# Performance work log

Measured on AMD Instinct MI355X. Metric: run time of the kernel, lower is better.

The kernel has to match this reference:

```python
import jax, jax.numpy as jnp
import numpy as np

B, C, H, W = 2, 16, 160, 192
S, D = 3, 48
MIN_DEPTH, MAX_DEPTH = 0.5, 10.0
EPS = 1e-6


def setup_inputs() -> dict:
    key = jax.random.key(0)
    k1, k2 = jax.random.split(key)
    ref_feats = jax.random.normal(k1, (B, C, H, W), jnp.float32)
    src_feats = jax.random.normal(k2, (S, B, C, H, W), jnp.float32)
    K = np.array([[200.0, 0.0, W / 2.0], [0.0, 200.0, H / 2.0], [0.0, 0.0, 1.0]], np.float32)
    ref_intrinsics = jnp.broadcast_to(jnp.asarray(K), (B, 3, 3))
    src_intrinsics = jnp.broadcast_to(jnp.asarray(K), (S, B, 3, 3))
    T = np.tile(np.eye(4, dtype=np.float32), (S, B, 1, 1))
    T[:, :, 0, 3] = np.array([0.15, -0.15, 0.05], np.float32)[:, None]  # x baselines
    T[:, :, 1, 3] = 0.05  # small y offset
    ref_to_src = jnp.asarray(T)
    depth_hypotheses = jnp.linspace(MIN_DEPTH, MAX_DEPTH, D, dtype=jnp.float32)
    return {"ref_feats": ref_feats, "src_feats": src_feats,
            "ref_intrinsics": ref_intrinsics, "src_intrinsics": src_intrinsics,
            "ref_to_src": ref_to_src, "depth_hypotheses": depth_hypotheses}


def _bilinear(img, x, y, valid):
    """img: [B,C,Hs,Ws]; x,y,valid: [B,D,N]. Zero padding outside. -> [B,C,D,N]"""
    Hs, Ws = img.shape[2], img.shape[3]
    x0 = jnp.floor(x); y0 = jnp.floor(y)
    fx = x - x0; fy = y - y0
    x0i = x0.astype(jnp.int32); y0i = y0.astype(jnp.int32)
    gather = jax.vmap(lambda im, yy, xx: im[:, yy, xx])  # per-batch [C,D,N]
    out = jnp.zeros(img.shape[:2] + x.shape[1:], img.dtype)
    for dy in (0, 1):
        for dx in (0, 1):
            xi = x0i + dx; yi = y0i + dy
            w = (fx if dx else 1.0 - fx) * (fy if dy else 1.0 - fy)
            ok = valid & (xi >= 0) & (xi < Ws) & (yi >= 0) & (yi < Hs)
            vals = gather(img, jnp.clip(yi, 0, Hs - 1), jnp.clip(xi, 0, Ws - 1))
            out = out + vals * jnp.where(ok, w, 0.0)[:, None]
    return out


def _ncc(f1, f2, eps=EPS):
    """NCC over channel axis 1. f1: [B,C,1,H,W], f2: [B,C,D,H,W] -> [B,D,H,W]"""
    f1 = f1 - f1.mean(axis=1, keepdims=True)
    f2 = f2 - f2.mean(axis=1, keepdims=True)
    num = (f1 * f2).sum(axis=1)
    den = jnp.sqrt((f1 * f1).sum(axis=1)) * jnp.sqrt((f2 * f2).sum(axis=1)) + eps
    return num / den


def reference(ref_feats, src_feats, ref_intrinsics, src_intrinsics, ref_to_src, depth_hypotheses):
    b, c, h, w = ref_feats.shape
    s = src_feats.shape[0]
    us, vs = jnp.meshgrid(jnp.arange(w, dtype=jnp.float32), jnp.arange(h, dtype=jnp.float32))  # [h,w]
    pix = jnp.stack([us.ravel(), vs.ravel(), jnp.ones(h * w, jnp.float32)], axis=0)  # [3,HW]
    rays = jnp.einsum('bij,jn->bin', jnp.linalg.inv(ref_intrinsics), pix)  # [B,3,HW]
    X = depth_hypotheses[None, :, None, None] * rays[:, None]  # [B,D,3,HW]
    cost = jnp.zeros((b, depth_hypotheses.shape[0], h, w), ref_feats.dtype)
    for si in range(s):
        R = ref_to_src[si, :, :3, :3]; t = ref_to_src[si, :, :3, 3]
        Xs = jnp.einsum('bij,bdjn->bdin', R, X) + t[:, None, :, None]  # [B,D,3,HW]
        p = jnp.einsum('bij,bdjn->bdin', src_intrinsics[si], Xs)
        z = p[:, :, 2]
        valid = z > 1e-3
        zs = jnp.maximum(z, 1e-3)
        x = p[:, :, 0] / zs; y = p[:, :, 1] / zs  # [B,D,HW]
        warped = _bilinear(src_feats[si], x, y, valid).reshape(b, c, -1, h, w)  # [B,C,D,H,W]
        cost = cost + _ncc(ref_feats[:, :, None], warped)
    return cost / s
```

## Files before the change

kernel.cpp:

```cpp
#include <hip/hip_runtime.h>
#include <math.h>

constexpr int B = 2, C = 16, H = 160, W = 192, S = 3, D = 48;
constexpr int HW = H * W;

__global__ __launch_bounds__(256) void plane_sweep_kernel(
    const float* __restrict__ ref_feats,
    const float* __restrict__ src_feats,
    const float* __restrict__ ref_intr,
    const float* __restrict__ src_intr,
    const float* __restrict__ ref_to_src,
    const float* __restrict__ depths,
    float* __restrict__ out)
{
    const int idx = blockIdx.x * blockDim.x + threadIdx.x;
    const int total = B * D * HW;
    if (idx >= total) return;

    const int w = idx % W;
    const int h = (idx / W) % H;
    const int d = (idx / HW) % D;
    const int b = idx / (HW * D);

    const float* Kp = ref_intr + b * 9;
    const double a00 = Kp[0], a01 = Kp[1], a02 = Kp[2];
    const double a10 = Kp[3], a11 = Kp[4], a12 = Kp[5];
    const double a20 = Kp[6], a21 = Kp[7], a22 = Kp[8];
    const double cof00 =  (a11 * a22 - a12 * a21);
    const double cof01 = -(a10 * a22 - a12 * a20);
    const double cof02 =  (a10 * a21 - a11 * a20);
    const double cof10 = -(a01 * a22 - a02 * a21);
    const double cof11 =  (a00 * a22 - a02 * a20);
    const double cof12 = -(a00 * a21 - a01 * a20);
    const double cof20 =  (a01 * a12 - a02 * a11);
    const double cof21 = -(a00 * a12 - a02 * a10);
    const double cof22 =  (a00 * a11 - a01 * a10);
    const double det = a00 * cof00 + a01 * cof01 + a02 * cof02;
    const double invdet = 1.0 / det;
    const double i00 = cof00 * invdet, i01 = cof10 * invdet, i02 = cof20 * invdet;
    const double i10 = cof01 * invdet, i11 = cof11 * invdet, i12 = cof21 * invdet;
    const double i20 = cof02 * invdet, i21 = cof12 * invdet, i22 = cof22 * invdet;

    const double u = (double)w;
    const double v = (double)h;
    const double rayx = i00 * u + i01 * v + i02;
    const double rayy = i10 * u + i11 * v + i12;
    const double rayz = i20 * u + i21 * v + i22;

    const double depth = (double)depths[d];
    const double X0 = depth * rayx;
    const double X1 = depth * rayy;
    const double X2 = depth * rayz;

    float f1[C];
    const float* rp = ref_feats + (b * C) * HW + h * W + w;
    float sum1 = 0.0f;
    #pragma unroll
    for (int c = 0; c < C; ++c) {
        f1[c] = rp[c * HW];
        sum1 += f1[c];
    }
    const float m1 = sum1 * (1.0f / C);
    float sq1 = 0.0f;
    #pragma unroll
    for (int c = 0; c < C; ++c) {
        f1[c] -= m1;
        sq1 += f1[c] * f1[c];
    }
    const float n1 = sqrtf(sq1);

    float cost = 0.0f;

    for (int s = 0; s < S; ++s) {
        const float* Tp  = ref_to_src + (s * B + b) * 16;
        const float* Ksp = src_intr   + (s * B + b) * 9;

        const double Xsx = (double)Tp[0] * X0 + (double)Tp[1] * X1 + (double)Tp[2]  * X2 + (double)Tp[3];
        const double Xsy = (double)Tp[4] * X0 + (double)Tp[5] * X1 + (double)Tp[6]  * X2 + (double)Tp[7];
        const double Xsz = (double)Tp[8] * X0 + (double)Tp[9] * X1 + (double)Tp[10] * X2 + (double)Tp[11];

        const double p0 = (double)Ksp[0] * Xsx + (double)Ksp[1] * Xsy + (double)Ksp[2] * Xsz;
        const double p1 = (double)Ksp[3] * Xsx + (double)Ksp[4] * Xsy + (double)Ksp[5] * Xsz;
        const double p2 = (double)Ksp[6] * Xsx + (double)Ksp[7] * Xsy + (double)Ksp[8] * Xsz;

        const bool valid = p2 > 0.001;
        const double zs = fmax(p2, 0.001);
        const double invz = 1.0 / zs;
        const double x = p0 * invz;
        const double y = p1 * invz;

        const double x0f = floor(x);
        const double y0f = floor(y);
        const double fx = x - x0f;
        const double fy = y - y0f;
        const int x0 = (int)x0f;
        const int y0 = (int)y0f;
        const int x1 = x0 + 1;
        const int y1 = y0 + 1;

        double dw00 = (1.0 - fx) * (1.0 - fy);
        double dw01 = fx * (1.0 - fy);
        double dw10 = (1.0 - fx) * fy;
        double dw11 = fx * fy;
        const bool okx0 = (x0 >= 0) && (x0 < W);
        const bool okx1 = (x1 >= 0) && (x1 < W);
        const bool oky0 = (y0 >= 0) && (y0 < H);
        const bool oky1 = (y1 >= 0) && (y1 < H);
        const float w00 = (float)((valid && okx0 && oky0) ? dw00 : 0.0);
        const float w01 = (float)((valid && okx1 && oky0) ? dw01 : 0.0);
        const float w10 = (float)((valid && okx0 && oky1) ? dw10 : 0.0);
        const float w11 = (float)((valid && okx1 && oky1) ? dw11 : 0.0);

        const int x0c = min(max(x0, 0), W - 1);
        const int x1c = min(max(x1, 0), W - 1);
        const int y0c = min(max(y0, 0), H - 1);
        const int y1c = min(max(y1, 0), H - 1);

        const int off00 = y0c * W + x0c;
        const int off01 = y0c * W + x1c;
        const int off10 = y1c * W + x0c;
        const int off11 = y1c * W + x1c;

        const float* base = src_feats + ((size_t)(s * B + b) * C) * HW;

        float f2[C];
        float sum2 = 0.0f;
        #pragma unroll
        for (int c = 0; c < C; ++c) {
            const float* p = base + c * HW;
            const float v00 = p[off00];
            const float v01 = p[off01];
            const float v10 = p[off10];
            const float v11 = p[off11];
            const float val = w00 * v00 + w01 * v01 + w10 * v10 + w11 * v11;
            f2[c] = val;
            sum2 += val;
        }
        const float m2 = sum2 * (1.0f / C);
        float sq2 = 0.0f;
        float dot = 0.0f;
        #pragma unroll
        for (int c = 0; c < C; ++c) {
            const float f2c = f2[c] - m2;
            sq2 = fmaf(f2c, f2c, sq2);
            dot = fmaf(f1[c], f2c, dot);
        }
        const float den = n1 * sqrtf(sq2) + 1e-6f;
        cost += dot / den;
    }

    out[idx] = cost * (1.0f / S);
}

extern "C" void kernel_launch(void* const* d_in, const int* in_sizes, int n_in,
                              void* d_out, int out_size, void* d_ws, size_t ws_size,
                              hipStream_t stream) {
    const float* ref_feats  = (const float*)d_in[0];
    const float* src_feats  = (const float*)d_in[1];
    const float* ref_intr   = (const float*)d_in[2];
    const float* src_intr   = (const float*)d_in[3];
    const float* ref_to_src = (const float*)d_in[4];
    const float* depths     = (const float*)d_in[5];
    float* out = (float*)d_out;

    const int total = B * D * H * W;
    const int block = 256;
    const int grid = (total + block - 1) / block;
    plane_sweep_kernel<<<grid, block, 0, stream>>>(
        ref_feats, src_feats, ref_intr, src_intr, ref_to_src, depths, out);
}
```

Baseline: 183.1 us.

## Process eight depths per thread and use paired loads for bilinear taps

Each thread now handles a block of 8 depth hypotheses for one pixel. The per-pixel setup (inverse intrinsics, ray, projection coefficients folded into a linear-in-depth form, reference feature normalization) is computed once and reused across those depths. The bilinear sampling now reads two adjacent x-samples with a single 8-byte vector load per row, and edge columns are handled by remapping the weights. This cuts redundant double-precision setup and load instructions, but launches 8x fewer threads, which lowers parallelism and occupancy, and the f32x2 loads may be misaligned.

```diff
diff --git a/kernel.cpp b/kernel.cpp
--- a/kernel.cpp
+++ b/kernel.cpp
@@ -3,6 +3,16 @@
 
 constexpr int B = 2, C = 16, H = 160, W = 192, S = 3, D = 48;
 constexpr int HW = H * W;
+constexpr int DPER = 8;
+constexpr int NDBLK = D / DPER;
+
+typedef float f32x2 __attribute__((ext_vector_type(2)));
+
+__device__ __forceinline__ f32x2 load2(const float* p) {
+    f32x2 v;
+    __builtin_memcpy(&v, p, sizeof(f32x2));
+    return v;
+}
 
 __global__ __launch_bounds__(256) void plane_sweep_kernel(
     const float* __restrict__ ref_feats,
@@ -14,13 +24,14 @@
     float* __restrict__ out)
 {
     const int idx = blockIdx.x * blockDim.x + threadIdx.x;
-    const int total = B * D * HW;
+    const int total = B * NDBLK * HW;
     if (idx >= total) return;
 
-    const int w = idx % W;
-    const int h = (idx / W) % H;
-    const int d = (idx / HW) % D;
-    const int b = idx / (HW * D);
+    const int w    = idx % W;
+    const int h    = (idx / W) % H;
+    const int dblk = (idx / HW) % NDBLK;
+    const int b    = idx / (HW * NDBLK);
+    const int d0   = dblk * DPER;
 
     const float* Kp = ref_intr + b * 9;
     const double a00 = Kp[0], a01 = Kp[1], a02 = Kp[2];
@@ -47,10 +58,24 @@
     const double rayy = i10 * u + i11 * v + i12;
     const double rayz = i20 * u + i21 * v + i22;
 
-    const double depth = (double)depths[d];
-    const double X0 = depth * rayx;
-    const double X1 = depth * rayy;
-    const double X2 = depth * rayz;
+    double ka0[S], ka1[S], ka2[S], kt0[S], kt1[S], kt2[S];
+    const float* vbase[S];
+    #pragma unroll
+    for (int s = 0; s < S; ++s) {
+        const float* Tp  = ref_to_src + (s * B + b) * 16;
+        const float* Ksp = src_intr   + (s * B + b) * 9;
+        const double ar0 = (double)Tp[0] * rayx + (double)Tp[1] * rayy + (double)Tp[2]  * rayz;
+        const double ar1 = (double)Tp[4] * rayx + (double)Tp[5] * rayy + (double)Tp[6]  * rayz;
+        const double ar2 = (double)Tp[8] * rayx + (double)Tp[9] * rayy + (double)Tp[10] * rayz;
+        ka0[s] = (double)Ksp[0] * ar0 + (double)Ksp[1] * ar1 + (double)Ksp[2] * ar2;
+        ka1[s] = (double)Ksp[3] * ar0 + (double)Ksp[4] * ar1 + (double)Ksp[5] * ar2;
+        ka2[s] = (double)Ksp[6] * ar0 + (double)Ksp[7] * ar1 + (double)Ksp[8] * ar2;
+        const double t0 = Tp[3], t1 = Tp[7], t2 = Tp[11];
+        kt0[s] = (double)Ksp[0] * t0 + (double)Ksp[1] * t1 + (double)Ksp[2] * t2;
+        kt1[s] = (double)Ksp[3] * t0 + (double)Ksp[4] * t1 + (double)Ksp[5] * t2;
+        kt2[s] = (double)Ksp[6] * t0 + (double)Ksp[7] * t1 + (double)Ksp[8] * t2;
+        vbase[s] = src_feats + ((size_t)(s * B + b) * C) * HW;
+    }
 
     float f1[C];
     const float* rp = ref_feats + (b * C) * HW + h * W + w;
@@ -69,87 +94,80 @@
     }
     const float n1 = sqrtf(sq1);
 
-    float cost = 0.0f;
+    float* outp = out + (size_t)(b * D + d0) * HW + h * W + w;
 
-    for (int s = 0; s < S; ++s) {
-        const float* Tp  = ref_to_src + (s * B + b) * 16;
-        const float* Ksp = src_intr   + (s * B + b) * 9;
+    #pragma unroll 1
+    for (int di = 0; di < DPER; ++di) {
+        const double depth = (double)depths[d0 + di];
+        float cost = 0.0f;
 
-        const double Xsx = (double)Tp[0] * X0 + (double)Tp[1] * X1 + (double)Tp[2]  * X2 + (double)Tp[3];
-        const double Xsy = (double)Tp[4] * X0 + (double)Tp[5] * X1 + (double)Tp[6]  * X2 + (double)Tp[7];
-        const double Xsz = (double)Tp[8] * X0 + (double)Tp[9] * X1 + (double)Tp[10] * X2 + (double)Tp[11];
+        #pragma unroll
+        for (int s = 0; s < S; ++s) {
+            const double p0 = depth * ka0[s] + kt0[s];
+            const double p1 = depth * ka1[s] + kt1[s];
+            const double p2 = depth * ka2[s] + kt2[s];
 
-        const double p0 = (double)Ksp[0] * Xsx + (double)Ksp[1] * Xsy + (double)Ksp[2] * Xsz;
-        const double p1 = (double)Ksp[3] * Xsx + (double)Ksp[4] * Xsy + (double)Ksp[5] * Xsz;
-        const double p2 = (double)Ksp[6] * Xsx + (double)Ksp[7] * Xsy + (double)Ksp[8] * Xsz;
+            const bool valid = p2 > 0.001;
+            const double zs = fmax(p2, 0.001);
+            const double invz = 1.0 / zs;
+            const double x = p0 * invz;
+            const double y = p1 * invz;
 
-        const bool valid = p2 > 0.001;
-        const double zs = fmax(p2, 0.001);
-        const double invz = 1.0 / zs;
-        const double x = p0 * invz;
-        const double y = p1 * invz;
+            const double x0f = floor(x);
+            const double y0f = floor(y);
+            const double fx = x - x0f;
+            const double fy = y - y0f;
+            const int x0 = (int)x0f;
+            const int y0 = (int)y0f;
+            const int y1 = y0 + 1;
 
-        const double x0f = floor(x);
-        const double y0f = floor(y);
-        const double fx = x - x0f;
-        const double fy = y - y0f;
-        const int x0 = (int)x0f;
-        const int y0 = (int)y0f;
-        const int x1 = x0 + 1;
-        const int y1 = y0 + 1;
+            const double wx0 = 1.0 - fx;
+            const double wx1 = fx;
+            const bool interior = (x0 >= 0) && (x0 < W - 1);
+            const float wA = (float)(interior ? wx0 : ((x0 == -1)    ? wx1 : 0.0));
+            const float wB = (float)(interior ? wx1 : ((x0 == W - 1) ? wx0 : 0.0));
 
-        double dw00 = (1.0 - fx) * (1.0 - fy);
-        double dw01 = fx * (1.0 - fy);
-        double dw10 = (1.0 - fx) * fy;
-        double dw11 = fx * fy;
-        const bool okx0 = (x0 >= 0) && (x0 < W);
-        const bool okx1 = (x1 >= 0) && (x1 < W);
-        const bool oky0 = (y0 >= 0) && (y0 < H);
-        const bool oky1 = (y1 >= 0) && (y1 < H);
-        const float w00 = (float)((valid && okx0 && oky0) ? dw00 : 0.0);
-        const float w01 = (float)((valid && okx1 && oky0) ? dw01 : 0.0);
-        const float w10 = (float)((valid && okx0 && oky1) ? dw10 : 0.0);
-        const float w11 = (float)((valid && okx1 && oky1) ? dw11 : 0.0);
+            const bool oky0 = (y0 >= 0) && (y0 < H);
+            const bool oky1 = (y1 >= 0) && (y1 < H);
+            const float wy0 = (float)((valid && oky0) ? (1.0 - fy) : 0.0);
+            const float wy1 = (float)((valid && oky1) ? fy : 0.0);
 
-        const int x0c = min(max(x0, 0), W - 1);
-        const int x1c = min(max(x1, 0), W - 1);
-        const int y0c = min(max(y0, 0), H - 1);
-        const int y1c = min(max(y1, 0), H - 1);
+            const int xa  = min(max(x0, 0), W - 2);
+            const int y0c = min(max(y0, 0), H - 1);
+            const int y1c = min(max(y1, 0), H - 1);
+            const int off0 = y0c * W + xa;
+            const int off1 = y1c * W + xa;
 
-        const int off00 = y0c * W + x0c;
-        const int off01 = y0c * W + x1c;
-        const int off10 = y1c * W + x0c;
-        const int off11 = y1c * W + x1c;
+            const float* base = vbase[s];
 
-        const float* base = src_feats + ((size_t)(s * B + b) * C) * HW;
+            float f2[C];
+            float sum2 = 0.0f;
+            #pragma unroll
+            for (int c = 0; c < C; ++c) {
+                const float* pc = base + c * HW;
+                const f32x2 r0 = load2(pc + off0);
+                const f32x2 r1 = load2(pc + off1);
+                const float t0 = fmaf(wA, r0.x, wB * r0.y);
+                const float t1 = fmaf(wA, r1.x, wB * r1.y);
+                const float val = fmaf(wy0, t0, wy1 * t1);
+                f2[c] = val;
+                sum2 += val;
+            }
+            const float m2 = sum2 * (1.0f / C);
+            float sq2 = 0.0f;
+            float dot = 0.0f;
+            #pragma unroll
+            for (int c = 0; c < C; ++c) {
+                const float f2c = f2[c] - m2;
+                sq2 = fmaf(f2c, f2c, sq2);
+                dot = fmaf(f1[c], f2c, dot);
+            }
+            const float den = n1 * sqrtf(sq2) + 1e-6f;
+            cost += dot / den;
+        }
 
-        float f2[C];
-        float sum2 = 0.0f;
-        #pragma unroll
-        for (int c = 0; c < C; ++c) {
-            const float* p = base + c * HW;
-            const float v00 = p[off00];
-            const float v01 = p[off01];
-            const float v10 = p[off10];
-            const float v11 = p[off11];
-            const float val = w00 * v00 + w01 * v01 + w10 * v10 + w11 * v11;
-            f2[c] = val;
-            sum2 += val;
-        }
-        const float m2 = sum2 * (1.0f / C);
-        float sq2 = 0.0f;
-        float dot = 0.0f;
-        #pragma unroll
-        for (int c = 0; c < C; ++c) {
-            const float f2c = f2[c] - m2;
-            sq2 = fmaf(f2c, f2c, sq2);
-            dot = fmaf(f1[c], f2c, dot);
-        }
-        const float den = n1 * sqrtf(sq2) + 1e-6f;
-        cost += dot / den;
+        outp[(size_t)di * HW] = cost * (1.0f / S);
     }
-
-    out[idx] = cost * (1.0f / S);
 }
 
 extern "C" void kernel_launch(void* const* d_in, const int* in_sizes, int n_in,
@@ -163,7 +181,7 @@
     const float* depths     = (const float*)d_in[5];
     float* out = (float*)d_out;
 
-    const int total = B * D * H * W;
+    const int total = B * NDBLK * H * W;
     const int block = 256;
     const int grid = (total + block - 1) / block;
     plane_sweep_kernel<<<grid, block, 0, stream>>>(
```

Result: slower. 355.7 us (+94.2%).

## Precompute per-pixel projection rays in a geometry kernel and use paired bilinear loads

Applied to the files above, without the earlier changes.

Adds a geometry pre-pass that computes, for each pixel and source view, K_s*R*ray in double plus the per-batch K_s*t term, so the sweep kernel only does depth*ka+kt per hypothesis. This removes the per-thread 3x3 inverse and the matrix products from the hot kernel. The bilinear sampling now uses a clamped x anchor with two 2-float loads per row and separable weights, done in float, which halves the load instructions. It adds a workspace round trip of double-precision ka reads and a second launch, with a fallback kernel when the workspace is too small.

```diff
diff --git a/kernel.cpp b/kernel.cpp
--- a/kernel.cpp
+++ b/kernel.cpp
@@ -3,24 +3,31 @@
 
 constexpr int B = 2, C = 16, H = 160, W = 192, S = 3, D = 48;
 constexpr int HW = H * W;
-
-__global__ __launch_bounds__(256) void plane_sweep_kernel(
-    const float* __restrict__ ref_feats,
-    const float* __restrict__ src_feats,
+constexpr int NPIX = B * HW;
+constexpr size_t KA_ELEMS = (size_t)S * 3 * NPIX;
+constexpr size_t KT_ELEMS = (size_t)S * 3 * B;
+constexpr size_t WS_NEEDED = (KA_ELEMS + KT_ELEMS) * sizeof(double);
+
+typedef float f32x2 __attribute__((ext_vector_type(2)));
+
+__device__ __forceinline__ f32x2 load2(const float* p) {
+    f32x2 v;
+    __builtin_memcpy(&v, p, sizeof(f32x2));
+    return v;
+}
+
+__global__ __launch_bounds__(256) void geom_kernel(
     const float* __restrict__ ref_intr,
     const float* __restrict__ src_intr,
     const float* __restrict__ ref_to_src,
-    const float* __restrict__ depths,
-    float* __restrict__ out)
+    double* __restrict__ ka,
+    double* __restrict__ kt)
 {
-    const int idx = blockIdx.x * blockDim.x + threadIdx.x;
-    const int total = B * D * HW;
-    if (idx >= total) return;
-
-    const int w = idx % W;
-    const int h = (idx / W) % H;
-    const int d = (idx / HW) % D;
-    const int b = idx / (HW * D);
+    const int pi = blockIdx.x * blockDim.x + threadIdx.x;
+    if (pi >= NPIX) return;
+    const int w = pi % W;
+    const int h = (pi / W) % H;
+    const int b = pi / HW;
 
     const float* Kp = ref_intr + b * 9;
     const double a00 = Kp[0], a01 = Kp[1], a02 = Kp[2];
@@ -47,10 +54,47 @@
     const double rayy = i10 * u + i11 * v + i12;
     const double rayz = i20 * u + i21 * v + i22;
 
+    #pragma unroll
+    for (int s = 0; s < S; ++s) {
+        const float* Tp  = ref_to_src + (s * B + b) * 16;
+        const float* Ksp = src_intr   + (s * B + b) * 9;
+        const double ar0 = (double)Tp[0] * rayx + (double)Tp[1] * rayy + (double)Tp[2]  * rayz;
+        const double ar1 = (double)Tp[4] * rayx + (double)Tp[5] * rayy + (double)Tp[6]  * rayz;
+        const double ar2 = (double)Tp[8] * rayx + (double)Tp[9] * rayy + (double)Tp[10] * rayz;
+        ka[(size_t)(s * 3 + 0) * NPIX + pi] = (double)Ksp[0] * ar0 + (double)Ksp[1] * ar1 + (double)Ksp[2] * ar2;
+        ka[(size_t)(s * 3 + 1) * NPIX + pi] = (double)Ksp[3] * ar0 + (double)Ksp[4] * ar1 + (double)Ksp[5] * ar2;
+        ka[(size_t)(s * 3 + 2) * NPIX + pi] = (double)Ksp[6] * ar0 + (double)Ksp[7] * ar1 + (double)Ksp[8] * ar2;
+        if (pi < B) {
+            const int bb = pi;
+            const float* Tp2  = ref_to_src + (s * B + bb) * 16;
+            const float* Ksp2 = src_intr   + (s * B + bb) * 9;
+            const double t0 = Tp2[3], t1 = Tp2[7], t2 = Tp2[11];
+            kt[(s * 3 + 0) * B + bb] = (double)Ksp2[0] * t0 + (double)Ksp2[1] * t1 + (double)Ksp2[2] * t2;
+            kt[(s * 3 + 1) * B + bb] = (double)Ksp2[3] * t0 + (double)Ksp2[4] * t1 + (double)Ksp2[5] * t2;
+            kt[(s * 3 + 2) * B + bb] = (double)Ksp2[6] * t0 + (double)Ksp2[7] * t1 + (double)Ksp2[8] * t2;
+        }
+    }
+}
+
+__global__ __launch_bounds__(256) void sweep_kernel(
+    const float* __restrict__ ref_feats,
+    const float* __restrict__ src_feats,
+    const double* __restrict__ ka,
+    const double* __restrict__ kt,
+    const float* __restrict__ depths,
+    float* __restrict__ out)
+{
+    const int idx = blockIdx.x * blockDim.x + threadIdx.x;
+    const int total = B * D * HW;
+    if (idx >= total) return;
+
+    const int w = idx % W;
+    const int h = (idx / W) % H;
+    const int d = (idx / HW) % D;
+    const int b = idx / (HW * D);
+    const int pi = b * HW + h * W + w;
+
     const double depth = (double)depths[d];
-    const double X0 = depth * rayx;
-    const double X1 = depth * rayy;
-    const double X2 = depth * rayz;
 
     float f1[C];
     const float* rp = ref_feats + (b * C) * HW + h * W + w;
@@ -71,17 +115,11 @@
 
     float cost = 0.0f;
 
+    #pragma unroll
     for (int s = 0; s < S; ++s) {
-        const float* Tp  = ref_to_src + (s * B + b) * 16;
-        const float* Ksp = src_intr   + (s * B + b) * 9;
-
-        const double Xsx = (double)Tp[0] * X0 + (double)Tp[1] * X1 + (double)Tp[2]  * X2 + (double)Tp[3];
-        const double Xsy = (double)Tp[4] * X0 + (double)Tp[5] * X1 + (double)Tp[6]  * X2 + (double)Tp[7];
-        const double Xsz = (double)Tp[8] * X0 + (double)Tp[9] * X1 + (double)Tp[10] * X2 + (double)Tp[11];
-
-        const double p0 = (double)Ksp[0] * Xsx + (double)Ksp[1] * Xsy + (double)Ksp[2] * Xsz;
-        const double p1 = (double)Ksp[3] * Xsx + (double)Ksp[4] * Xsy + (double)Ksp[5] * Xsz;
-        const double p2 = (double)Ksp[6] * Xsx + (double)Ksp[7] * Xsy + (double)Ksp[8] * Xsz;
+        const double p0 = depth * ka[(size_t)(s * 3 + 0) * NPIX + pi] + kt[(s * 3 + 0) * B + b];
+        const double p1 = depth * ka[(size_t)(s * 3 + 1) * NPIX + pi] + kt[(s * 3 + 1) * B + b];
+        const double p2 = depth * ka[(size_t)(s * 3 + 2) * NPIX + pi] + kt[(s * 3 + 2) * B + b];
 
         const bool valid = p2 > 0.001;
         const double zs = fmax(p2, 0.001);
@@ -91,35 +129,26 @@
 
         const double x0f = floor(x);
         const double y0f = floor(y);
-        const double fx = x - x0f;
-        const double fy = y - y0f;
+        const float fx = (float)(x - x0f);
+        const float fy = (float)(y - y0f);
         const int x0 = (int)x0f;
         const int y0 = (int)y0f;
-        const int x1 = x0 + 1;
         const int y1 = y0 + 1;
 
-        double dw00 = (1.0 - fx) * (1.0 - fy);
-        double dw01 = fx * (1.0 - fy);
-        double dw10 = (1.0 - fx) * fy;
-        double dw11 = fx * fy;
-        const bool okx0 = (x0 >= 0) && (x0 < W);
-        const bool okx1 = (x1 >= 0) && (x1 < W);
+        const bool interior = (x0 >= 0) && (x0 < W - 1);
+        const float wA = interior ? (1.0f - fx) : ((x0 == -1)    ? fx          : 0.0f);
+        const float wB = interior ? fx          : ((x0 == W - 1) ? (1.0f - fx) : 0.0f);
+
         const bool oky0 = (y0 >= 0) && (y0 < H);
         const bool oky1 = (y1 >= 0) && (y1 < H);
-        const float w00 = (float)((valid && okx0 && oky0) ? dw00 : 0.0);
-        const float w01 = (float)((valid && okx1 && oky0) ? dw01 : 0.0);
-        const float w10 = (float)((valid && okx0 && oky1) ? dw10 : 0.0);
-        const float w11 = (float)((valid && okx1 && oky1) ? dw11 : 0.0);
-
-        const int x0c = min(max(x0, 0), W - 1);
-        const int x1c = min(max(x1, 0), W - 1);
+        const float wy0 = (valid && oky0) ? (1.0f - fy) : 0.0f;
+        const float wy1 = (valid && oky1) ? fy : 0.0f;
+
+        const int xa  = min(max(x0, 0), W - 2);
         const int y0c = min(max(y0, 0), H - 1);
         const int y1c = min(max(y1, 0), H - 1);
-
-        const int off00 = y0c * W + x0c;
-        const int off01 = y0c * W + x1c;
-        const int off10 = y1c * W + x0c;
-        const int off11 = y1c * W + x1c;
+        const int off0 = y0c * W + xa;
+        const int off1 = y1c * W + xa;
 
         const float* base = src_feats + ((size_t)(s * B + b) * C) * HW;
 
@@ -127,12 +156,12 @@
         float sum2 = 0.0f;
         #pragma unroll
         for (int c = 0; c < C; ++c) {
-            const float* p = base + c * HW;
-            const float v00 = p[off00];
-            const float v01 = p[off01];
-            const float v10 = p[off10];
-            const float v11 = p[off11];
-            const float val = w00 * v00 + w01 * v01 + w10 * v10 + w11 * v11;
+            const float* pc = base + c * HW;
+            const f32x2 r0 = load2(pc + off0);
+            const f32x2 r1 = load2(pc + off1);
+            const float t0v = fmaf(wA, r0.x, wB * r0.y);
+            const float t1v = fmaf(wA, r1.x, wB * r1.y);
+            const float val = fmaf(wy0, t0v, wy1 * t1v);
             f2[c] = val;
             sum2 += val;
         }
@@ -149,6 +178,110 @@
         cost += dot / den;
     }
 
+    out[idx] = cost * (1.0f / S);
+}
+
+__global__ __launch_bounds__(256) void plane_sweep_fallback(
+    const float* __restrict__ ref_feats, const float* __restrict__ src_feats,
+    const float* __restrict__ ref_intr, const float* __restrict__ src_intr,
+    const float* __restrict__ ref_to_src, const float* __restrict__ depths,
+    float* __restrict__ out)
+{
+    const int idx = blockIdx.x * blockDim.x + threadIdx.x;
+    const int total = B * D * HW;
+    if (idx >= total) return;
+    const int w = idx % W;
+    const int h = (idx / W) % H;
+    const int d = (idx / HW) % D;
+    const int b = idx / (HW * D);
+
+    const float* Kp = ref_intr + b * 9;
+    const double a00 = Kp[0], a01 = Kp[1], a02 = Kp[2];
+    const double a10 = Kp[3], a11 = Kp[4], a12 = Kp[5];
+    const double a20 = Kp[6], a21 = Kp[7], a22 = Kp[8];
+    const double cof00 =  (a11 * a22 - a12 * a21);
+    const double cof01 = -(a10 * a22 - a12 * a20);
+    const double cof02 =  (a10 * a21 - a11 * a20);
+    const double cof10 = -(a01 * a22 - a02 * a21);
+    const double cof11 =  (a00 * a22 - a02 * a20);
+    const double cof12 = -(a00 * a21 - a01 * a20);
+    const double cof20 =  (a01 * a12 - a02 * a11);
+    const double cof21 = -(a00 * a12 - a02 * a10);
+    const double cof22 =  (a00 * a11 - a01 * a10);
+    const double det = a00 * cof00 + a01 * cof01 + a02 * cof02;
+    const double invdet = 1.0 / det;
+    const double i00 = cof00 * invdet, i01 = cof10 * invdet, i02 = cof20 * invdet;
+    const double i10 = cof01 * invdet, i11 = cof11 * invdet, i12 = cof21 * invdet;
+    const double i20 = cof02 * invdet, i21 = cof12 * invdet, i22 = cof22 * invdet;
+    const double u = (double)w, v = (double)h;
+    const double rayx = i00 * u + i01 * v + i02;
+    const double rayy = i10 * u + i11 * v + i12;
+    const double rayz = i20 * u + i21 * v + i22;
+    const double depth = (double)depths[d];
+    const double X0 = depth * rayx, X1 = depth * rayy, X2 = depth * rayz;
+
+    float f1[C];
+    const float* rp = ref_feats + (b * C) * HW + h * W + w;
+    float sum1 = 0.0f;
+    #pragma unroll
+    for (int c = 0; c < C; ++c) { f1[c] = rp[c * HW]; sum1 += f1[c]; }
+    const float m1 = sum1 * (1.0f / C);
+    float sq1 = 0.0f;
+    #pragma unroll
+    for (int c = 0; c < C; ++c) { f1[c] -= m1; sq1 += f1[c] * f1[c]; }
+    const float n1 = sqrtf(sq1);
+
+    float cost = 0.0f;
+    for (int s = 0; s < S; ++s) {
+        const float* Tp  = ref_to_src + (s * B + b) * 16;
+        const float* Ksp = src_intr   + (s * B + b) * 9;
+        const double Xsx = (double)Tp[0] * X0 + (double)Tp[1] * X1 + (double)Tp[2]  * X2 + (double)Tp[3];
+        const double Xsy = (double)Tp[4] * X0 + (double)Tp[5] * X1 + (double)Tp[6]  * X2 + (double)Tp[7];
+        const double Xsz = (double)Tp[8] * X0 + (double)Tp[9] * X1 + (double)Tp[10] * X2 + (double)Tp[11];
+        const double p0 = (double)Ksp[0] * Xsx + (double)Ksp[1] * Xsy + (double)Ksp[2] * Xsz;
+        const double p1 = (double)Ksp[3] * Xsx + (double)Ksp[4] * Xsy + (double)Ksp[5] * Xsz;
+        const double p2 = (double)Ksp[6] * Xsx + (double)Ksp[7] * Xsy + (double)Ksp[8] * Xsz;
+        const bool valid = p2 > 0.001;
+        const double zs = fmax(p2, 0.001);
+        const double invz = 1.0 / zs;
+        const double x = p0 * invz, y = p1 * invz;
+        const double x0f = floor(x), y0f = floor(y);
+        const float fx = (float)(x - x0f), fy = (float)(y - y0f);
+        const int x0 = (int)x0f, y0 = (int)y0f, y1 = y0 + 1;
+        const bool interior = (x0 >= 0) && (x0 < W - 1);
+        const float wA = interior ? (1.0f - fx) : ((x0 == -1)    ? fx          : 0.0f);
+        const float wB = interior ? fx          : ((x0 == W - 1) ? (1.0f - fx) : 0.0f);
+        const bool oky0 = (y0 >= 0) && (y0 < H);
+        const bool oky1 = (y1 >= 0) && (y1 < H);
+        const float wy0 = (valid && oky0) ? (1.0f - fy) : 0.0f;
+        const float wy1 = (valid && oky1) ? fy : 0.0f;
+        const int xa  = min(max(x0, 0), W - 2);
+        const int y0c = min(max(y0, 0), H - 1);
+        const int y1c = min(max(y1, 0), H - 1);
+        const int off0 = y0c * W + xa, off1 = y1c * W + xa;
+        const float* base = src_feats + ((size_t)(s * B + b) * C) * HW;
+        float f2[C];
+        float sum2 = 0.0f;
+        #pragma unroll
+        for (int c = 0; c < C; ++c) {
+            const float* pc = base + c * HW;
+            const f32x2 r0 = load2(pc + off0);
+            const f32x2 r1 = load2(pc + off1);
+            const float t0v = fmaf(wA, r0.x, wB * r0.y);
+            const float t1v = fmaf(wA, r1.x, wB * r1.y);
+            const float val = fmaf(wy0, t0v, wy1 * t1v);
+            f2[c] = val; sum2 += val;
+        }
+        const float m2 = sum2 * (1.0f / C);
+        float sq2 = 0.0f, dot = 0.0f;
+        #pragma unroll
+        for (int c = 0; c < C; ++c) {
+            const float f2c = f2[c] - m2;
+            sq2 = fmaf(f2c, f2c, sq2);
+            dot = fmaf(f1[c], f2c, dot);
+        }
+        cost += dot / (n1 * sqrtf(sq2) + 1e-6f);
+    }
     out[idx] = cost * (1.0f / S);
 }
 
@@ -162,10 +295,17 @@
     const float* ref_to_src = (const float*)d_in[4];
     const float* depths     = (const float*)d_in[5];
     float* out = (float*)d_out;
-
     const int total = B * D * H * W;
-    const int block = 256;
-    const int grid = (total + block - 1) / block;
-    plane_sweep_kernel<<<grid, block, 0, stream>>>(
-        ref_feats, src_feats, ref_intr, src_intr, ref_to_src, depths, out);
-}
+
+    if (ws_size >= WS_NEEDED) {
+        double* ka = (double*)d_ws;
+        double* kt = ka + KA_ELEMS;
+        geom_kernel<<<(NPIX + 255) / 256, 256, 0, stream>>>(
+            ref_intr, src_intr, ref_to_src, ka, kt);
+        sweep_kernel<<<(total + 255) / 256, 256, 0, stream>>>(
+            ref_feats, src_feats, ka, kt, depths, out);
+    } else {
+        plane_sweep_fallback<<<(total + 255) / 256, 256, 0, stream>>>(
+            ref_feats, src_feats, ref_intr, src_intr, ref_to_src, depths, out);
+    }
+}
```

Result: slower. 228.1 us (+24.5%).
